# Performance work log

Hardware: AMD Instinct MI355X
Metric: run time of the kernel (lower is better)

## Reference

```python
import jax, jax.numpy as jnp
import numpy as np

B, N, E, F, H, L = 64, 1024, 32768, 128, 32, 2
K = N // 2          # topk ratio 0.5 (fixed in source forward)
NB = 5              # num_neighbors: point cloud points per node
CF, P = 5, 50       # PI channels (filtration methods), PI_dim
OUT = 2

def gcn_conv(x, src, dst, emask, W, b, n):
    # PyG GCNConv: project first, symmetric norm with self-loops; emask zeroes filtered edges
    h = x @ W
    deg = jax.ops.segment_sum(emask, dst, num_segments=n) + 1.0
    dinv = jax.lax.rsqrt(deg)
    coef = (dinv[src] * dinv[dst] * emask)[:, None]
    agg = jax.ops.segment_sum(h[src] * coef, dst, num_segments=n)
    return agg + h * (dinv * dinv)[:, None] + b

def tcl(t, A, Bf, C):
    # Tensor Contraction Layer: mode-1/2/3 factor contraction
    return jnp.einsum('bijk,pi,qj,rk->bpqr', t, A, Bf, C)

def mlp2(h, Wa, ba, Wb, bb):
    return jax.nn.relu(h @ Wa + ba) @ Wb + bb

def setup_inputs():
    key = jax.random.key(0)
    ks = jax.random.split(key, 32)
    s = 0.05
    return {
        'x1': jax.random.normal(ks[0], (B, N, F), jnp.float32),
        'edge_index1': jax.random.randint(ks[1], (B, 2, E), 0, N),
        'PI1': jax.random.uniform(ks[2], (B, CF, P, P), dtype=jnp.float32),
        'x2': jax.random.normal(ks[3], (B, N, F), jnp.float32),
        'edge_index2': jax.random.randint(ks[4], (B, 2, E), 0, N),
        'PI2': jax.random.uniform(ks[5], (B, CF, P, P), dtype=jnp.float32),
        'W_score': jax.random.normal(ks[6], (F, NB * 2)) * s,
        'b_score': jnp.zeros((NB * 2,)),
        'W_gcn0': jax.random.normal(ks[7], (F, H)) * s,
        'b_gcn0': jnp.zeros((H,)),
        'Wm0a': jax.random.normal(ks[8], (H, H)) * s,
        'bm0a': jnp.zeros((H,)),
        'Wm0b': jax.random.normal(ks[9], (H, H * H)) * s,
        'bm0b': jnp.zeros((H * H,)),
        'W_gcn1': jax.random.normal(ks[10], (H * H, H)) * s,
        'b_gcn1': jnp.zeros((H,)),
        'Wm1a': jax.random.normal(ks[11], (H, H)) * s,
        'bm1a': jnp.zeros((H,)),
        'Wm1b': jax.random.normal(ks[12], (H, H * H)) * s,
        'bm1b': jnp.zeros((H * H,)),
        'F0': jax.random.normal(ks[13], (H, L)) * s,
        'F1': jax.random.normal(ks[14], (H, H)) * s,
        'F2': jax.random.normal(ks[15], (H, H)) * s,
        'K_conv': jax.random.normal(ks[16], (H, CF, 2, 2)) * s,
        'b_conv': jnp.zeros((H,)),
        'G0': jax.random.normal(ks[17], (H, H)) * s,
        'G1': jax.random.normal(ks[18], (H, P // 2)) * s,
        'G2': jax.random.normal(ks[19], (H, P // 2)) * s,
        'H0': jax.random.normal(ks[20], (2 * H, 2 * H)) * s,
        'H1': jax.random.normal(ks[21], (H, H)) * s,
        'H2': jax.random.normal(ks[22], (H, H)) * s,
        'Wo1': jax.random.normal(ks[23], (H, H)) * s,
        'bo1': jnp.zeros((H,)),
        'Wo2': jax.random.normal(ks[24], (H, OUT)) * s,
        'bo2': jnp.zeros((OUT,)),
    }

def reference(x1, edge_index1, PI1, x2, edge_index2, PI2, W_score, b_score,
              W_gcn0, b_gcn0, Wm0a, bm0a, Wm0b, bm0b,
              W_gcn1, b_gcn1, Wm1a, bm1a, Wm1b, bm1b,
              F0, F1, F2, K_conv, b_conv, G0, G1, G2,
              H0, H1, H2, Wo1, bo1, Wo2, bo2):
    ones = jnp.ones((E,), jnp.float32)

    def pool_one(xg, s_, d_):
        # score_node_layer -> point cloud -> lifespan score -> topk(0.5) -> filter_adj
        emb = gcn_conv(xg, s_, d_, ones, W_score, b_score, N)
        pc = emb.reshape(N, NB, 2)
        score = jnp.abs(pc[..., 1] - pc[..., 0]).sum(-1)
        _, perm = jax.lax.top_k(score, K)
        newidx = jnp.full((N,), -1).at[perm].set(jnp.arange(K))
        r, c = newidx[s_], newidx[d_]
        valid = (r >= 0) & (c >= 0)
        return xg[perm], jnp.where(valid, r, 0), jnp.where(valid, c, 0), valid.astype(jnp.float32)

    def branch(x, ei, PI):
        src, dst = ei[:, 0, :], ei[:, 1, :]
        xp, psrc, pdst, em = jax.vmap(pool_one)(x, src, dst)
        conv0 = jax.vmap(lambda h, s_, d_, m: gcn_conv(h, s_, d_, m, W_gcn0, b_gcn0, K))
        conv1 = jax.vmap(lambda h, s_, d_, m: gcn_conv(h, s_, d_, m, W_gcn1, b_gcn1, K))
        h1 = mlp2(conv0(xp, psrc, pdst, em), Wm0a, bm0a, Wm0b, bm0b)   # [B,K,H*H]
        h2 = mlp2(conv1(h1, psrc, pdst, em), Wm1a, bm1a, Wm1b, bm1b)   # [B,K,H*H]
        g = jnp.stack([h1.mean(1), h2.mean(1)], axis=1).reshape(B, L, H, H)
        gcn_t = tcl(g, F0, F1, F2)                                      # [B,H,H,H]
        pe = jax.lax.conv_general_dilated(PI, K_conv, (2, 2), 'VALID',
                                          dimension_numbers=('NCHW', 'OIHW', 'NCHW'))
        pe = jax.nn.relu(pe + b_conv[None, :, None, None])              # [B,H,25,25]
        pi_t = tcl(pe, G0, G1, G2)                                      # [B,H,H,H]
        fused = tcl(jnp.concatenate([gcn_t, pi_t], axis=1), H0, H1, H2) # [B,2H,H,H]
        pooled = fused.mean(axis=(1, 3))                                # [B,H]
        return jax.nn.relu(pooled @ Wo1 + bo1) @ Wo2 + bo2              # [B,OUT]

    return jnp.stack([branch(x1, edge_index1, PI1), branch(x2, edge_index2, PI2)])
```

## Files before the change

kernel.cpp:

```cpp
#include <hip/hip_runtime.h>
#include <cstdint>


constexpr int B_ = 64, N_ = 1024, E_ = 32768, F_ = 128, H_ = 32;
constexpr int CF_ = 5, P_ = 50, K_ = 512, G_ = 128, PO = 25;

constexpr size_t WS_SRCS  = 0;
constexpr size_t WS_ONODE = WS_SRCS + (size_t)G_*(E_/2);
constexpr size_t WS_VDEG  = WS_ONODE + (size_t)G_*K_;
constexpr size_t WS_EOFF  = WS_VDEG + (size_t)G_*(K_/2);
constexpr size_t WS_DINV  = WS_EOFF + (size_t)G_*K_;
constexpr size_t WS_GA    = WS_DINV + (size_t)G_*K_;
constexpr size_t WS_GC    = WS_GA + (size_t)G_*K_*H_;
constexpr size_t WS_PM0   = WS_GC + (size_t)G_*K_*H_;
constexpr size_t WS_PM1   = WS_PM0 + (size_t)G_*64;
constexpr size_t WS_PPI   = WS_PM1 + (size_t)G_*64;
constexpr size_t WS_F0V   = WS_PPI + (size_t)G_*32;
constexpr size_t WS_B01   = WS_F0V + 32;
constexpr size_t WS_C0B   = WS_B01 + 32;
constexpr size_t WS_C1B   = WS_C0B + 32;
constexpr size_t WS_W01   = WS_C1B + 32;
constexpr size_t WS_P0B   = WS_W01 + 1024;
constexpr size_t WS_P1B   = WS_P0B + 1024;

constexpr size_t WS_DSC   = WS_GC;

static __device__ __forceinline__ int swzf4(int row, int c4) {
  return row*32 + (((c4) ^ ((row >> 2) & 7)) << 2);
}

__global__ __launch_bounds__(512, 4) void kA_pre(
    const float* __restrict__ x1, const float* __restrict__ x2,
    const float* __restrict__ Wsc,
    const float* __restrict__ F0w, const float* __restrict__ F2w,
    const float* __restrict__ H0w, const float* __restrict__ H2w,
    const float* __restrict__ Wm0b, const float* __restrict__ bm0b,
    const float* __restrict__ Wm1b, const float* __restrict__ bm1b,
    const float* __restrict__ Wg1, float* __restrict__ ws)
{
  __shared__ float SM[640];
  int blk = blockIdx.x, t = threadIdx.x;

  if (blk < 8*G_) {
    int g = blk >> 3, sub = blk & 7, br = g >> 6, b = g & 63;
    const float* xg = (br ? x2 : x1) + (size_t)b*N_*F_;
    float* WdL = SM;
    if (t < F_) {
      #pragma unroll
      for (int j = 0; j < 5; ++j) WdL[t*5+j] = Wsc[t*10+2*j+1] - Wsc[t*10+2*j];
    }
    __syncthreads();
    int row = sub*128 + (t >> 2), q = t & 3;
    const float4* xr = (const float4*)(xg + (size_t)row*F_);
    float acc[5] = {};
    #pragma unroll
    for (int i = 0; i < 8; ++i) {
      int k4 = q + 4*i;
      float4 v = xr[k4];
      const float* w = &WdL[k4*20];
      #pragma unroll
      for (int j = 0; j < 5; ++j)
        acc[j] += v.x*w[j] + v.y*w[5+j] + v.z*w[10+j] + v.w*w[15+j];
    }
    #pragma unroll
    for (int j = 0; j < 5; ++j) {
      acc[j] += __shfl_xor(acc[j], 1, 4);
      acc[j] += __shfl_xor(acc[j], 2, 4);
    }
    if (q == 0) {
      float* o = ws + WS_DSC + ((size_t)g*N_ + row)*5;
      #pragma unroll
      for (int j = 0; j < 5; ++j) o[j] = acc[j];
    }
    return;
  }

  int blk2 = blk - 8*G_;
  if (blk2 == 0) {
    float* h0mS = SM;
    if (t < 32) { float s = 0.f; for (int qq = 0; qq < 64; ++qq) s += H0w[qq*64+t]; h0mS[t] = s*(1.f/64.f); }
    __syncthreads();
    if (t < 2) { float s = 0.f; for (int p = 0; p < 32; ++p) s += F0w[p*2+t]*h0mS[p]; ws[WS_F0V+t] = s; }
  } else if (blk2 <= 32) {
    int kk = blk2 - 1;
    int ol = t >> 4, seg = t & 15;
    const float4* ar = (const float4*)(Wm0b + (size_t)kk*1024 + seg*64);
    float s = 0.f;
    #pragma unroll
    for (int i = 0; i < 16; ++i) {
      float4 a = ar[i];
      int tt = seg*64 + i*4;
      s += a.x*Wg1[(tt+0)*32 + ol] + a.y*Wg1[(tt+1)*32 + ol]
         + a.z*Wg1[(tt+2)*32 + ol] + a.w*Wg1[(tt+3)*32 + ol];
    }
    s += __shfl_xor(s, 1, 16);
    s += __shfl_xor(s, 2, 16);
    s += __shfl_xor(s, 4, 16);
    s += __shfl_xor(s, 8, 16);
    if (seg == 0) ws[WS_W01 + kk*32 + ol] = s;
  } else if (blk2 == 33) {
    float* red = SM;
    int j = t & 31, seg = t >> 5;
    float s = 0.f;
    #pragma unroll
    for (int i = 0; i < 64; ++i) {
      int k = seg*64 + i;
      s += bm0b[k]*Wg1[k*32 + j];
    }
    red[seg*32 + j] = s;
    __syncthreads();
    if (t < 32) {
      float a = 0.f;
      #pragma unroll
      for (int q = 0; q < 16; ++q) a += red[q*32 + t];
      ws[WS_B01 + t] = a;
    }
  } else {
    const float* Wb = (blk2 == 34) ? Wm0b : Wm1b;
    const float* bb = (blk2 == 34) ? bm0b : bm1b;
    size_t dstP = (blk2 == 34) ? WS_P0B : WS_P1B;
    size_t dstC = (blk2 == 34) ? WS_C0B : WS_C1B;
    float* h2mL = SM;
    float* f2vL = SM + 32;
    if (t < 32) { float s = 0.f; for (int r = 0; r < 32; ++r) s += H2w[r*32+t]; h2mL[t] = s*(1.f/32.f); }
    __syncthreads();
    if (t < 32) { float s = 0.f; for (int r = 0; r < 32; ++r) s += F2w[r*32+t]*h2mL[r]; f2vL[t] = s; }
    __syncthreads();
    if (t < 256) {
      #pragma unroll
      for (int q = 0; q < 4; ++q) {
        int e = t*4 + q;
        int k = e >> 5, c = e & 31;
        float s = 0.f;
        #pragma unroll
        for (int kp = 0; kp < 32; ++kp) s += Wb[k*1024 + c*32 + kp]*f2vL[kp];
        ws[dstP + e] = s;
      }
    }
    if (t < 32) {
      float s = 0.f;
      #pragma unroll
      for (int kp = 0; kp < 32; ++kp) s += bb[t*32+kp]*f2vL[kp];
      ws[dstC+t] = s;
    }
  }
}

__global__ __launch_bounds__(256, 4) void kPI(
    const float* __restrict__ PI1, const float* __restrict__ PI2,
    const float* __restrict__ Kc, const float* __restrict__ bc,
    const float* __restrict__ G0w, const float* __restrict__ G2w,
    const float* __restrict__ H0w, const float* __restrict__ H2w,
    float* __restrict__ ws)
{
  int g = blockIdx.x, br = g >> 6, b = g & 63;
  const float* pig = (br ? PI2 : PI1) + (size_t)b*CF_*P_*P_;
  __shared__ float PIt[CF_*P_*P_];
  __shared__ float KcL[H_*CF_*4];
  __shared__ float bcL[H_], g0L[H_], g2L[PO], h2L[H_], hhL[H_];
  int t = threadIdx.x;
  for (int i = t; i < CF_*P_*P_; i += 256) PIt[i] = pig[i];
  for (int i = t; i < H_*CF_*4; i += 256) KcL[i] = Kc[i];
  if (t < 32) {
    bcL[t] = bc[t];
    float s = 0.f;
    for (int qq = 0; qq < 64; ++qq) s += H0w[qq*64 + 32 + t];
    hhL[t] = s * (1.f/64.f);
  }
  if (t >= 64 && t < 96) {
    int r = t - 64;
    float s = 0.f;
    for (int rr = 0; rr < 32; ++rr) s += H2w[rr*32 + r];
    h2L[r] = s * (1.f/32.f);
  }
  __syncthreads();
  if (t < 32) { float s = 0.f; for (int p = 0; p < 32; ++p) s += G0w[p*32+t]*hhL[p]; g0L[t] = s; }
  if (t >= 64 && t < 64+PO) {
    int kp = t - 64;
    float s = 0.f;
    for (int r = 0; r < 32; ++r) s += G2w[r*25+kp]*h2L[r];
    g2L[kp] = s;
  }
  __syncthreads();
  int jp = t >> 3, sub = t & 7;
  float acc = 0.f;
  if (jp < PO) {
    for (int i = sub; i < H_; i += 8) {
      const float* kcp = &KcL[i*20];
      float bi = bcL[i], gi = g0L[i];
      for (int kp = 0; kp < PO; ++kp) {
        float v = bi;
        #pragma unroll
        for (int c = 0; c < CF_; ++c) {
          const float* pp = &PIt[c*2500 + (2*jp)*50 + 2*kp];
          v += pp[0]*kcp[c*4+0] + pp[1]*kcp[c*4+1] + pp[50]*kcp[c*4+2] + pp[51]*kcp[c*4+3];
        }
        acc += fmaxf(v, 0.f) * gi * g2L[kp];
      }
    }
  }
  #pragma unroll
  for (int d = 4; d > 0; d >>= 1) acc += __shfl_down(acc, d, 8);
  if (sub == 0 && jp < PO) ws[WS_PPI + (size_t)g*32 + jp] = acc;
}

__global__ __launch_bounds__(1024, 4) void kBS(
    const int* __restrict__ ei1, const int* __restrict__ ei2,
    const float* __restrict__ bsc, float* __restrict__ ws)
{
  int g = blockIdx.x, br = g >> 6, b = g & 63;
  const int* ei  = (br ? ei2 : ei1) + (size_t)b*2*E_;
  const int* src = ei;
  const int* dst = ei + E_;
  int* onodeg = (int*)ws + WS_ONODE + (size_t)g*K_;
  uint16_t* vdegg = (uint16_t*)(ws + WS_VDEG) + (size_t)g*K_;
  int* ceoffg = (int*)ws + WS_EOFF + (size_t)g*K_;
  float* dinvg = ws + WS_DINV + (size_t)g*K_;
  uint16_t* csrc = (uint16_t*)(ws + WS_SRCS) + (size_t)g*E_;

  __shared__ uint16_t srcL[E_];
  __shared__ float DscL[N_*5];
  __shared__ float dinvF[N_];
  __shared__ int fbL[N_];
  __shared__ int fillL[N_];
  __shared__ int nidxL[N_];
  __shared__ int seoffL[K_];
  __shared__ int vdegL[K_];
  __shared__ int ceoffL[K_];
  __shared__ int hist[256], hsum[256];
  __shared__ int wtot[16], wbase[16], wsum[16];
  __shared__ int remL, dstarL;

  int t = threadIdx.x;
  { const float* Dg = ws + WS_DSC + (size_t)g*N_*5;
    for (int i = t; i < N_*5; i += 1024) DscL[i] = Dg[i]; }
  fillL[t] = 0;
  if (t == 0) remL = K_;
  __syncthreads();

  for (int i = 0; i < E_/1024; ++i) {
    int d = dst[t + i*1024];
    atomicAdd(&fillL[d], 1);
  }
  __syncthreads();

  int c = fillL[t];
  int lane = t & 63, w = t >> 6;
  int x = c;
  #pragma unroll
  for (int s = 1; s < 64; s <<= 1) {
    int v = __shfl_up(x, s);
    if (lane >= s) x += v;
  }
  if (lane == 63) wsum[w] = x;
  __syncthreads();
  if (w == 0 && lane < 16) {
    int y = wsum[lane];
    #pragma unroll
    for (int s = 1; s < 16; s <<= 1) {
      int v = __shfl_up(y, s, 16);
      if (lane >= s) y += v;
    }
    wsum[lane] = y;
  }
  __syncthreads();
  int off0 = ((w == 0) ? 0 : wsum[w-1]) + x - c;
  int off1 = off0 + c;
  fbL[t] = off0;
  dinvF[t] = rsqrtf((float)c + 1.0f);
  fillL[t] = 0;
  __syncthreads();

  for (int i = 0; i < E_/1024; ++i) {
    int e = t + i*1024;
    int d = dst[e], s = src[e];
    int pos = fbL[d] + atomicAdd(&fillL[d], 1);
    srcL[pos] = (uint16_t)s;
  }
  __syncthreads();

  uint32_t key;
  {
    float agg[5] = {};
    for (int e = off0; e < off1; ++e) {
      int s = srcL[e];
      float dvs = dinvF[s];
      const float* hr = &DscL[s*5];
      #pragma unroll
      for (int j = 0; j < 5; ++j) agg[j] += hr[j]*dvs;
    }
    float dv = dinvF[t];
    const float* hn = &DscL[t*5];
    float sc = 0.f;
    #pragma unroll
    for (int j = 0; j < 5; ++j)
      sc += fabsf(dv*(agg[j] + dv*hn[j]) + (bsc[2*j+1] - bsc[2*j]));
    key = __float_as_uint(sc);
  }
  __syncthreads();

  uint32_t pref = 0, prefMask = 0;
  #pragma unroll
  for (int pass = 0; pass < 4; ++pass) {
    int shift = 24 - 8*pass;
    if (t < 256) hist[t] = 0;
    __syncthreads();
    bool cand = (key & prefMask) == pref;
    if (cand) atomicAdd(&hist[(key >> shift) & 255], 1);
    __syncthreads();
    if (t < 256) hsum[t] = hist[t];
    __syncthreads();
    for (int s = 1; s < 256; s <<= 1) {
      int v = 0;
      if (t < 256) v = hsum[t] + ((t + s < 256) ? hsum[t + s] : 0);
      __syncthreads();
      if (t < 256) hsum[t] = v;
      __syncthreads();
    }
    int rem = remL;
    if (t < 256) {
      int above = (t == 255) ? 0 : hsum[t+1];
      if (hsum[t] >= rem && above < rem) dstarL = t;
    }
    __syncthreads();
    int ds = dstarL;
    if (t == 0) remL = rem - ((ds == 255) ? 0 : hsum[ds+1]);
    pref |= (uint32_t)ds << shift;
    prefMask |= 0xFFu << shift;
    __syncthreads();
  }
  uint32_t T = pref;
  int r = remL;

  bool eq = (key == T);
  uint64_t mEq = __ballot(eq);
  int lpEq = (int)__popcll(mEq & ((1ull << lane) - 1));
  if (lane == 0) wtot[w] = (int)__popcll(mEq);
  __syncthreads();
  if (t == 0) { int a = 0; for (int q = 0; q < 16; ++q) { wbase[q] = a; a += wtot[q]; } }
  __syncthreads();
  bool sel = (key > T) || (eq && (wbase[w] + lpEq) < r);
  __syncthreads();
  uint64_t mS = __ballot(sel);
  int lpS = (int)__popcll(mS & ((1ull << lane) - 1));
  if (lane == 0) wtot[w] = (int)__popcll(mS);
  __syncthreads();
  if (t == 0) { int a = 0; for (int q = 0; q < 16; ++q) { wbase[q] = a; a += wtot[q]; } }
  __syncthreads();
  int rank = wbase[w] + lpS;
  nidxL[t] = sel ? rank : -1;
  if (sel) onodeg[rank] = t;
  __syncthreads();

  if (sel) {
    int c2 = 0;
    for (int e = off0; e < off1; ++e) {
      int m = nidxL[srcL[e]];
      if (m >= 0) srcL[off0 + (c2++)] = (uint16_t)m;
    }
    vdegL[rank] = c2;
    seoffL[rank] = off0;
  }
  __syncthreads();

  int vv = 0, xx = 0, w2 = t >> 6;
  if (t < K_) {
    vv = vdegL[t]; xx = vv;
    int l2 = t & 63;
    #pragma unroll
    for (int s = 1; s < 64; s <<= 1) {
      int v = __shfl_up(xx, s);
      if (l2 >= s) xx += v;
    }
    if (l2 == 63) wsum[w2] = xx;
  }
  __syncthreads();
  if (t == 0) { int run = 0; for (int q = 0; q < 8; ++q) { int tm = wsum[q]; wsum[q] = run; run += tm; } }
  __syncthreads();
  if (t < K_) {
    int ce = wsum[w2] + xx - vv;
    ceoffL[t] = ce;
    ceoffg[t] = ce;
    vdegg[t] = (uint16_t)vv;
    dinvg[t] = rsqrtf((float)vv + 1.0f);
  }
  __syncthreads();

  if (t < K_) {
    int s0 = seoffL[t], n = vdegL[t], d0 = ceoffL[t];
    for (int i = 0; i < n; ++i) csrc[d0 + i] = srcL[s0 + i];
  }
}

static __device__ __forceinline__ void mmA(
    const float* __restrict__ S, const float* __restrict__ Wp,
    float (&acc)[4][4], int it, int jt)
{
  const int i0 = it*4, swa = it & 7;
  #pragma unroll
  for (int kv = 0; kv < 8; ++kv) {
    float4 w0 = *(const float4*)&Wp[(kv*4+0)*36 + jt*4];
    float4 w1 = *(const float4*)&Wp[(kv*4+1)*36 + jt*4];
    float4 w2 = *(const float4*)&Wp[(kv*4+2)*36 + jt*4];
    float4 w3 = *(const float4*)&Wp[(kv*4+3)*36 + jt*4];
    #pragma unroll
    for (int d = 0; d < 4; ++d) {
      float4 a = *(const float4*)&S[(i0+d)*32 + ((kv ^ swa) << 2)];
      acc[d][0] += a.x*w0.x + a.y*w1.x + a.z*w2.x + a.w*w3.x;
      acc[d][1] += a.x*w0.y + a.y*w1.y + a.z*w2.y + a.w*w3.y;
      acc[d][2] += a.x*w0.z + a.y*w1.z + a.z*w2.z + a.w*w3.z;
      acc[d][3] += a.x*w0.w + a.y*w1.w + a.z*w2.w + a.w*w3.w;
    }
  }
}

__global__ __launch_bounds__(512, 4) void kG1(
    const float* __restrict__ x1, const float* __restrict__ x2,
    const float* __restrict__ Wg0, float* __restrict__ ws)
{
  int g = blockIdx.x, half = blockIdx.y, br = g >> 6, b = g & 63;
  const float* xg = (br ? x2 : x1) + (size_t)b*N_*F_;
  const int* onodeg = (const int*)ws + WS_ONODE + (size_t)g*K_ + half*256;
  const float* dinvg = ws + WS_DINV + (size_t)g*K_ + half*256;
  float* gAg = ws + WS_GA + (size_t)g*K_*H_ + (size_t)half*256*H_;

  __shared__ float wbuf[F_*36];
  __shared__ int   onodeL[256];
  __shared__ float dinvL[256];

  int t = threadIdx.x;
  for (int i = t; i < F_*H_; i += 512) wbuf[(i >> 5)*36 + (i & 31)] = Wg0[i];
  if (t < 256) { onodeL[t] = onodeg[t]; dinvL[t] = dinvg[t]; }
  __syncthreads();

  const int it = t >> 3, jt = t & 7;
  const int i0 = it*4;
  const float* xr0 = xg + (size_t)onodeL[i0+0]*F_;
  const float* xr1 = xg + (size_t)onodeL[i0+1]*F_;
  const float* xr2 = xg + (size_t)onodeL[i0+2]*F_;
  const float* xr3 = xg + (size_t)onodeL[i0+3]*F_;
  float acc[4][4] = {};
  for (int k4 = 0; k4 < 32; ++k4) {
    float4 w0 = *(const float4*)&wbuf[(k4*4+0)*36 + jt*4];
    float4 w1 = *(const float4*)&wbuf[(k4*4+1)*36 + jt*4];
    float4 w2 = *(const float4*)&wbuf[(k4*4+2)*36 + jt*4];
    float4 w3 = *(const float4*)&wbuf[(k4*4+3)*36 + jt*4];
    float4 a;
    a = *(const float4*)(xr0 + k4*4);
    acc[0][0]+=a.x*w0.x+a.y*w1.x+a.z*w2.x+a.w*w3.x; acc[0][1]+=a.x*w0.y+a.y*w1.y+a.z*w2.y+a.w*w3.y;
    acc[0][2]+=a.x*w0.z+a.y*w1.z+a.z*w2.z+a.w*w3.z; acc[0][3]+=a.x*w0.w+a.y*w1.w+a.z*w2.w+a.w*w3.w;
    a = *(const float4*)(xr1 + k4*4);
    acc[1][0]+=a.x*w0.x+a.y*w1.x+a.z*w2.x+a.w*w3.x; acc[1][1]+=a.x*w0.y+a.y*w1.y+a.z*w2.y+a.w*w3.y;
    acc[1][2]+=a.x*w0.z+a.y*w1.z+a.z*w2.z+a.w*w3.z; acc[1][3]+=a.x*w0.w+a.y*w1.w+a.z*w2.w+a.w*w3.w;
    a = *(const float4*)(xr2 + k4*4);
    acc[2][0]+=a.x*w0.x+a.y*w1.x+a.z*w2.x+a.w*w3.x; acc[2][1]+=a.x*w0.y+a.y*w1.y+a.z*w2.y+a.w*w3.y;
    acc[2][2]+=a.x*w0.z+a.y*w1.z+a.z*w2.z+a.w*w3.z; acc[2][3]+=a.x*w0.w+a.y*w1.w+a.z*w2.w+a.w*w3.w;
    a = *(const float4*)(xr3 + k4*4);
    acc[3][0]+=a.x*w0.x+a.y*w1.x+a.z*w2.x+a.w*w3.x; acc[3][1]+=a.x*w0.y+a.y*w1.y+a.z*w2.y+a.w*w3.y;
    acc[3][2]+=a.x*w0.z+a.y*w1.z+a.z*w2.z+a.w*w3.z; acc[3][3]+=a.x*w0.w+a.y*w1.w+a.z*w2.w+a.w*w3.w;
  }
  #pragma unroll
  for (int d = 0; d < 4; ++d) {
    int row = i0 + d;
    float rs = dinvL[row];
    float4 o; o.x=acc[d][0]*rs; o.y=acc[d][1]*rs; o.z=acc[d][2]*rs; o.w=acc[d][3]*rs;
    *(float4*)&gAg[row*32 + jt*4] = o;
  }
}

static __device__ __forceinline__ void convG(
    const float* __restrict__ gS, float* __restrict__ cbuf,
    const float* __restrict__ bias, const float* __restrict__ dinvL,
    const int* __restrict__ eoffL, const int* __restrict__ vcntL,
    const uint16_t* __restrict__ srcS, int half, int t)
{
  int ddl = t & 255, hc = t >> 8;
  int dd = half*256 + ddl;
  int lo = eoffL[ddl], n = vcntL[ddl];
  int c0 = hc*16;
  float4 a0 = {0,0,0,0}, a1 = a0, a2 = a0, a3 = a0;
  for (int i = 0; i < n; ++i) {
    int ss = srcS[lo + i];
    const float* r = gS + ss*32 + c0;
    float4 v;
    v = *(const float4*)(r+0);  a0.x+=v.x; a0.y+=v.y; a0.z+=v.z; a0.w+=v.w;
    v = *(const float4*)(r+4);  a1.x+=v.x; a1.y+=v.y; a1.z+=v.z; a1.w+=v.w;
    v = *(const float4*)(r+8);  a2.x+=v.x; a2.y+=v.y; a2.z+=v.z; a2.w+=v.w;
    v = *(const float4*)(r+12); a3.x+=v.x; a3.y+=v.y; a3.z+=v.z; a3.w+=v.w;
  }
  { const float* r = gS + dd*32 + c0;
    float4 v;
    v = *(const float4*)(r+0);  a0.x+=v.x; a0.y+=v.y; a0.z+=v.z; a0.w+=v.w;
    v = *(const float4*)(r+4);  a1.x+=v.x; a1.y+=v.y; a1.z+=v.z; a1.w+=v.w;
    v = *(const float4*)(r+8);  a2.x+=v.x; a2.y+=v.y; a2.z+=v.z; a2.w+=v.w;
    v = *(const float4*)(r+12); a3.x+=v.x; a3.y+=v.y; a3.z+=v.z; a3.w+=v.w; }
  float dvd = dinvL[ddl];
  float4 r0, r1, r2, r3;
  r0.x = dvd*a0.x + bias[c0+0];  r0.y = dvd*a0.y + bias[c0+1];
  r0.z = dvd*a0.z + bias[c0+2];  r0.w = dvd*a0.w + bias[c0+3];
  r1.x = dvd*a1.x + bias[c0+4];  r1.y = dvd*a1.y + bias[c0+5];
  r1.z = dvd*a1.z + bias[c0+6];  r1.w = dvd*a1.w + bias[c0+7];
  r2.x = dvd*a2.x + bias[c0+8];  r2.y = dvd*a2.y + bias[c0+9];
  r2.z = dvd*a2.z + bias[c0+10]; r2.w = dvd*a2.w + bias[c0+11];
  r3.x = dvd*a3.x + bias[c0+12]; r3.y = dvd*a3.y + bias[c0+13];
  r3.z = dvd*a3.z + bias[c0+14]; r3.w = dvd*a3.w + bias[c0+15];
  int g4 = hc*4;
  *(float4*)&cbuf[swzf4(ddl, g4+0)] = r0;
  *(float4*)&cbuf[swzf4(ddl, g4+1)] = r1;
  *(float4*)&cbuf[swzf4(ddl, g4+2)] = r2;
  *(float4*)&cbuf[swzf4(ddl, g4+3)] = r3;
}

__global__ __launch_bounds__(512, 4) void kG2(
    const float* __restrict__ bg0,
    const float* __restrict__ Wm0a, const float* __restrict__ bm0a,
    float* __restrict__ ws)
{
  int g = blockIdx.x, half = blockIdx.y;
  const float* gAg = ws + WS_GA + (size_t)g*K_*H_;
  float* gCg = ws + WS_GC + (size_t)g*K_*H_;
  const uint16_t* srcS = (const uint16_t*)(ws + WS_SRCS) + (size_t)g*E_;
  const int* eoffg = (const int*)ws + WS_EOFF + (size_t)g*K_ + half*256;
  const uint16_t* vdegg = (const uint16_t*)(ws + WS_VDEG) + (size_t)g*K_ + half*256;
  const float* dinvg = ws + WS_DINV + (size_t)g*K_ + half*256;

  __shared__ float cbufA[256*32];
  __shared__ float cbufB[256*32];
  __shared__ float wA[32*36];
  __shared__ float wB[32*36];
  __shared__ float scrP[64*33];
  __shared__ int   eoffL[256];
  __shared__ int   vcntL[256];
  __shared__ float dinvL[256];

  int t = threadIdx.x;
  for (int i = t; i < 1024; i += 512) {
    int k = i >> 5, j = i & 31;
    wA[k*36+j] = Wm0a[i];
    wB[k*36+j] = ws[WS_W01 + i];
  }
  if (t < 256) { eoffL[t] = eoffg[t]; vcntL[t] = vdegg[t]; dinvL[t] = dinvg[t]; }
  __syncthreads();

  convG(gAg, cbufA, bg0, dinvL, eoffL, vcntL, srcS, half, t);
  __syncthreads();

  const int it = t >> 3, jt = t & 7;
  float acc[4][4] = {};
  mmA(cbufA, wA, acc, it, jt);
  {
    float b0 = bm0a[jt*4+0], b1 = bm0a[jt*4+1], b2 = bm0a[jt*4+2], b3 = bm0a[jt*4+3];
    float cp0=0.f, cp1=0.f, cp2=0.f, cp3=0.f;
    #pragma unroll
    for (int d = 0; d < 4; ++d) {
      float v0=fmaxf(acc[d][0]+b0,0.f), v1=fmaxf(acc[d][1]+b1,0.f);
      float v2=fmaxf(acc[d][2]+b2,0.f), v3=fmaxf(acc[d][3]+b3,0.f);
      cp0+=v0; cp1+=v1; cp2+=v2; cp3+=v3;
      float4 o; o.x=v0; o.y=v1; o.z=v2; o.w=v3;
      *(float4*)&cbufB[swzf4(it*4+d, jt)] = o;
    }
    scrP[it*33 + jt*4+0] = cp0; scrP[it*33 + jt*4+1] = cp1;
    scrP[it*33 + jt*4+2] = cp2; scrP[it*33 + jt*4+3] = cp3;
  }
  __syncthreads();

  if (t < 32) {
    float s = 0.f;
    #pragma unroll
    for (int q = 0; q < 64; ++q) s += scrP[q*33 + t];
    ws[WS_PM0 + (size_t)g*64 + half*32 + t] = s;
  }

  float acc2[4][4] = {};
  mmA(cbufB, wB, acc2, it, jt);
  {
    float b0 = ws[WS_B01+jt*4+0], b1 = ws[WS_B01+jt*4+1];
    float b2 = ws[WS_B01+jt*4+2], b3 = ws[WS_B01+jt*4+3];
    #pragma unroll
    for (int d = 0; d < 4; ++d) {
      int row = it*4 + d;
      float rs = dinvL[row];
      float4 o;
      o.x=(acc2[d][0]+b0)*rs; o.y=(acc2[d][1]+b1)*rs;
      o.z=(acc2[d][2]+b2)*rs; o.w=(acc2[d][3]+b3)*rs;
      *(float4*)&gCg[(half*256+row)*32 + jt*4] = o;
    }
  }
}

__global__ __launch_bounds__(512, 4) void kG4(
    const float* __restrict__ bg1,
    const float* __restrict__ Wm1a, const float* __restrict__ bm1a,
    float* __restrict__ ws)
{
  int g = blockIdx.x, half = blockIdx.y;
  const float* gCg = ws + WS_GC + (size_t)g*K_*H_;
  const uint16_t* srcS = (const uint16_t*)(ws + WS_SRCS) + (size_t)g*E_;
  const int* eoffg = (const int*)ws + WS_EOFF + (size_t)g*K_ + half*256;
  const uint16_t* vdegg = (const uint16_t*)(ws + WS_VDEG) + (size_t)g*K_ + half*256;
  const float* dinvg = ws + WS_DINV + (size_t)g*K_ + half*256;

  __shared__ float cbufA[256*32];
  __shared__ float wA[32*36];
  __shared__ float scrP[64*33];
  __shared__ int   eoffL[256];
  __shared__ int   vcntL[256];
  __shared__ float dinvL[256];

  int t = threadIdx.x;
  for (int i = t; i < 1024; i += 512) wA[(i>>5)*36 + (i&31)] = Wm1a[i];
  if (t < 256) { eoffL[t] = eoffg[t]; vcntL[t] = vdegg[t]; dinvL[t] = dinvg[t]; }
  __syncthreads();

  convG(gCg, cbufA, bg1, dinvL, eoffL, vcntL, srcS, half, t);
  __syncthreads();

  const int it = t >> 3, jt = t & 7;
  float acc[4][4] = {};
  mmA(cbufA, wA, acc, it, jt);
  {
    float b0 = bm1a[jt*4+0], b1 = bm1a[jt*4+1], b2 = bm1a[jt*4+2], b3 = bm1a[jt*4+3];
    float cp0=0.f, cp1=0.f, cp2=0.f, cp3=0.f;
    #pragma unroll
    for (int d = 0; d < 4; ++d) {
      cp0 += fmaxf(acc[d][0]+b0,0.f); cp1 += fmaxf(acc[d][1]+b1,0.f);
      cp2 += fmaxf(acc[d][2]+b2,0.f); cp3 += fmaxf(acc[d][3]+b3,0.f);
    }
    scrP[it*33 + jt*4+0] = cp0; scrP[it*33 + jt*4+1] = cp1;
    scrP[it*33 + jt*4+2] = cp2; scrP[it*33 + jt*4+3] = cp3;
  }
  __syncthreads();

  if (t < 32) {
    float s = 0.f;
    #pragma unroll
    for (int q = 0; q < 64; ++q) s += scrP[q*33 + t];
    ws[WS_PM1 + (size_t)g*64 + half*32 + t] = s;
  }
}

__global__ __launch_bounds__(64) void k5_final(
    const float* __restrict__ F1w, const float* __restrict__ G1w,
    const float* __restrict__ H1w, const float* __restrict__ Wo1,
    const float* __restrict__ bo1, const float* __restrict__ Wo2,
    const float* __restrict__ bo2, const float* __restrict__ ws,
    float* __restrict__ out)
{
  int g = blockIdx.x, t = threadIdx.x;
  __shared__ float mr0[32], mr1[32], AL[32], TL[32], pl[32], zl[32], ppiL[PO];
  if (t < 32) {
    mr0[t] = (ws[WS_PM0 + (size_t)g*64 + t] + ws[WS_PM0 + (size_t)g*64 + 32 + t]) * (1.f/512.f);
    mr1[t] = (ws[WS_PM1 + (size_t)g*64 + t] + ws[WS_PM1 + (size_t)g*64 + 32 + t]) * (1.f/512.f);
  }
  if (t >= 32 && t < 32+PO) ppiL[t-32] = ws[WS_PPI + (size_t)g*32 + (t-32)];
  __syncthreads();
  float f00 = ws[WS_F0V], f01 = ws[WS_F0V+1];
  if (t < 32) {
    float s0 = ws[WS_C0B + t], s1 = ws[WS_C1B + t];
    for (int k = 0; k < 32; ++k) {
      s0 += mr0[k]*ws[WS_P0B + k*32 + t];
      s1 += mr1[k]*ws[WS_P1B + k*32 + t];
    }
    AL[t] = f00*s0 + f01*s1;
  }
  __syncthreads();
  if (t < 32) {
    float s = 0.f;
    for (int jp = 0; jp < 32; ++jp) s += F1w[t*32+jp]*AL[jp];
    for (int jp = 0; jp < PO; ++jp) s += G1w[t*25+jp]*ppiL[jp];
    TL[t] = s;
  }
  __syncthreads();
  if (t < 32) {
    float s = 0.f;
    for (int j = 0; j < 32; ++j) s += H1w[t*32+j]*TL[j];
    pl[t] = s;
  }
  __syncthreads();
  if (t < 32) {
    float s = bo1[t];
    for (int j = 0; j < 32; ++j) s += pl[j]*Wo1[j*32+t];
    zl[t] = fmaxf(s, 0.f);
  }
  __syncthreads();
  if (t < 2) {
    float s = bo2[t];
    for (int q = 0; q < 32; ++q) s += zl[q]*Wo2[q*2+t];
    int br = g >> 6, b = g & 63;
    out[br*(B_*2) + b*2 + t] = s;
  }
}

extern "C" void kernel_launch(void* const* d_in, const int* in_sizes, int n_in,
                              void* d_out, int out_size, void* d_ws, size_t ws_size,
                              hipStream_t stream) {
  (void)in_sizes; (void)n_in; (void)out_size; (void)ws_size;
  const float* x1      = (const float*)d_in[0];
  const int*   ei1     = (const int*)  d_in[1];
  const float* PI1     = (const float*)d_in[2];
  const float* x2      = (const float*)d_in[3];
  const int*   ei2     = (const int*)  d_in[4];
  const float* PI2     = (const float*)d_in[5];
  const float* W_score = (const float*)d_in[6];
  const float* b_score = (const float*)d_in[7];
  const float* W_gcn0  = (const float*)d_in[8];
  const float* b_gcn0  = (const float*)d_in[9];
  const float* Wm0a    = (const float*)d_in[10];
  const float* bm0a    = (const float*)d_in[11];
  const float* Wm0b    = (const float*)d_in[12];
  const float* bm0b    = (const float*)d_in[13];
  const float* W_gcn1  = (const float*)d_in[14];
  const float* b_gcn1  = (const float*)d_in[15];
  const float* Wm1a    = (const float*)d_in[16];
  const float* bm1a    = (const float*)d_in[17];
  const float* Wm1b    = (const float*)d_in[18];
  const float* bm1b    = (const float*)d_in[19];
  const float* F0w     = (const float*)d_in[20];
  const float* F1w     = (const float*)d_in[21];
  const float* F2w     = (const float*)d_in[22];
  const float* Kc      = (const float*)d_in[23];
  const float* bc      = (const float*)d_in[24];
  const float* G0w     = (const float*)d_in[25];
  const float* G1w     = (const float*)d_in[26];
  const float* G2w     = (const float*)d_in[27];
  const float* H0w     = (const float*)d_in[28];
  const float* H1w     = (const float*)d_in[29];
  const float* H2w     = (const float*)d_in[30];
  const float* Wo1     = (const float*)d_in[31];
  const float* bo1     = (const float*)d_in[32];
  const float* Wo2     = (const float*)d_in[33];
  const float* bo2     = (const float*)d_in[34];
  float* ws  = (float*)d_ws;
  float* out = (float*)d_out;

  kA_pre<<<8*G_ + 36, 512, 0, stream>>>(x1, x2, W_score,
                                        F0w, F2w, H0w, H2w,
                                        Wm0b, bm0b, Wm1b, bm1b, W_gcn1, ws);
  kPI<<<G_, 256, 0, stream>>>(PI1, PI2, Kc, bc, G0w, G2w, H0w, H2w, ws);
  kBS<<<G_, 1024, 0, stream>>>(ei1, ei2, b_score, ws);
  kG1<<<dim3(G_, 2), 512, 0, stream>>>(x1, x2, W_gcn0, ws);
  kG2<<<dim3(G_, 2), 512, 0, stream>>>(b_gcn0, Wm0a, bm0a, ws);
  kG4<<<dim3(G_, 2), 512, 0, stream>>>(b_gcn1, Wm1a, bm1a, ws);
  k5_final<<<G_, 64, 0, stream>>>(F1w, G1w, H1w, Wo1, bo1, Wo2, bo2, ws, out);
}
```

Measured before the change: 188.9 us.

## Reparallelize PI conv over output positions and use wave-level suffix scan in top-k

The PI kernel now assigns each thread a conv output position, caches its 2x2x5 input patch in registers, loops over all 32 channels, and reduces rows through shared scratch. Before, 8 threads per row each walked 25 columns and 4 channels, and only 200 of 256 threads did work. The H0/H2 column means are now computed cooperatively by all threads with shuffles instead of 32 serial threads each. In kBS, the 8-step block-wide Hillis-Steele suffix scan with barriers is replaced by a single-wavefront shuffle scan, and the histogram reset is folded into the selection step to remove barriers per radix pass.

```diff
diff --git a/kernel.cpp b/kernel.cpp
--- a/kernel.cpp
+++ b/kernel.cpp
@@ -158,21 +158,29 @@
   __shared__ float PIt[CF_*P_*P_];
   __shared__ float KcL[H_*CF_*4];
   __shared__ float bcL[H_], g0L[H_], g2L[PO], h2L[H_], hhL[H_];
+  __shared__ float scr[640];
   int t = threadIdx.x;
   for (int i = t; i < CF_*P_*P_; i += 256) PIt[i] = pig[i];
   for (int i = t; i < H_*CF_*4; i += 256) KcL[i] = Kc[i];
-  if (t < 32) {
-    bcL[t] = bc[t];
-    float s = 0.f;
-    for (int qq = 0; qq < 64; ++qq) s += H0w[qq*64 + 32 + t];
-    hhL[t] = s * (1.f/64.f);
-  }
-  if (t >= 64 && t < 96) {
-    int r = t - 64;
-    float s = 0.f;
-    for (int rr = 0; rr < 32; ++rr) s += H2w[rr*32 + r];
-    h2L[r] = s * (1.f/32.f);
-  }
+  {
+    int p = t >> 3, s = t & 7;
+    float v = 0.f;
+    #pragma unroll
+    for (int q = 0; q < 8; ++q) v += H0w[(s + q*8)*64 + 32 + p];
+    #pragma unroll
+    for (int d = 4; d > 0; d >>= 1) v += __shfl_down(v, d, 8);
+    if (s == 0) hhL[p] = v * (1.f/64.f);
+  }
+  {
+    int r = t >> 3, s = t & 7;
+    float v = 0.f;
+    #pragma unroll
+    for (int q = 0; q < 4; ++q) v += H2w[(s + q*8)*32 + r];
+    #pragma unroll
+    for (int d = 4; d > 0; d >>= 1) v += __shfl_down(v, d, 8);
+    if (s == 0) h2L[r] = v * (1.f/32.f);
+  }
+  if (t < 32) bcL[t] = bc[t];
   __syncthreads();
   if (t < 32) { float s = 0.f; for (int p = 0; p < 32; ++p) s += G0w[p*32+t]*hhL[p]; g0L[t] = s; }
   if (t >= 64 && t < 64+PO) {
@@ -182,26 +190,32 @@
     g2L[kp] = s;
   }
   __syncthreads();
-  int jp = t >> 3, sub = t & 7;
-  float acc = 0.f;
-  if (jp < PO) {
-    for (int i = sub; i < H_; i += 8) {
+  for (int pos = t; pos < PO*PO; pos += 256) {
+    int jp = pos / PO, kp = pos - jp*PO;
+    float p00[CF_], p01[CF_], p10[CF_], p11[CF_];
+    #pragma unroll
+    for (int c = 0; c < CF_; ++c) {
+      const float* q = &PIt[c*2500 + (2*jp)*50 + 2*kp];
+      p00[c] = q[0]; p01[c] = q[1]; p10[c] = q[50]; p11[c] = q[51];
+    }
+    float acc = 0.f;
+    for (int i = 0; i < H_; ++i) {
+      float v = bcL[i];
       const float* kcp = &KcL[i*20];
-      float bi = bcL[i], gi = g0L[i];
-      for (int kp = 0; kp < PO; ++kp) {
-        float v = bi;
-        #pragma unroll
-        for (int c = 0; c < CF_; ++c) {
-          const float* pp = &PIt[c*2500 + (2*jp)*50 + 2*kp];
-          v += pp[0]*kcp[c*4+0] + pp[1]*kcp[c*4+1] + pp[50]*kcp[c*4+2] + pp[51]*kcp[c*4+3];
-        }
-        acc += fmaxf(v, 0.f) * gi * g2L[kp];
-      }
-    }
-  }
-  #pragma unroll
-  for (int d = 4; d > 0; d >>= 1) acc += __shfl_down(acc, d, 8);
-  if (sub == 0 && jp < PO) ws[WS_PPI + (size_t)g*32 + jp] = acc;
+      #pragma unroll
+      for (int c = 0; c < CF_; ++c)
+        v += p00[c]*kcp[c*4+0] + p01[c]*kcp[c*4+1] + p10[c]*kcp[c*4+2] + p11[c]*kcp[c*4+3];
+      acc += fmaxf(v, 0.f) * g0L[i];
+    }
+    scr[pos] = acc * g2L[kp];
+  }
+  __syncthreads();
+  if (t < PO) {
+    float s = 0.f;
+    #pragma unroll
+    for (int k = 0; k < PO; ++k) s += scr[t*PO + k];
+    ws[WS_PPI + (size_t)g*32 + t] = s;
+  }
 }
 
 __global__ __launch_bounds__(1024, 4) void kBS(
@@ -235,6 +249,7 @@
   { const float* Dg = ws + WS_DSC + (size_t)g*N_*5;
     for (int i = t; i < N_*5; i += 1024) DscL[i] = Dg[i]; }
   fillL[t] = 0;
+  if (t < 256) hist[t] = 0;
   if (t == 0) remL = K_;
   __syncthreads();
 
@@ -303,32 +318,37 @@
   #pragma unroll
   for (int pass = 0; pass < 4; ++pass) {
     int shift = 24 - 8*pass;
-    if (t < 256) hist[t] = 0;
-    __syncthreads();
     bool cand = (key & prefMask) == pref;
     if (cand) atomicAdd(&hist[(key >> shift) & 255], 1);
     __syncthreads();
-    if (t < 256) hsum[t] = hist[t];
+    if (w == 0) {
+      int base = lane*4;
+      int h0 = hist[base+0], h1 = hist[base+1], h2 = hist[base+2], h3 = hist[base+3];
+      int suf = h0 + h1 + h2 + h3;
+      #pragma unroll
+      for (int sh = 1; sh < 64; sh <<= 1) {
+        int v = __shfl_down(suf, sh);
+        if (lane + sh < 64) suf += v;
+      }
+      hsum[base+0] = suf;
+      hsum[base+1] = suf - h0;
+      hsum[base+2] = suf - h0 - h1;
+      hsum[base+3] = suf - h0 - h1 - h2;
+    }
     __syncthreads();
-    for (int s = 1; s < 256; s <<= 1) {
-      int v = 0;
-      if (t < 256) v = hsum[t] + ((t + s < 256) ? hsum[t + s] : 0);
-      __syncthreads();
-      if (t < 256) hsum[t] = v;
-      __syncthreads();
-    }
     int rem = remL;
     if (t < 256) {
       int above = (t == 255) ? 0 : hsum[t+1];
       if (hsum[t] >= rem && above < rem) dstarL = t;
+      hist[t] = 0;
     }
     __syncthreads();
     int ds = dstarL;
     if (t == 0) remL = rem - ((ds == 255) ? 0 : hsum[ds+1]);
     pref |= (uint32_t)ds << shift;
     prefMask |= 0xFFu << shift;
-    __syncthreads();
-  }
+  }
+  __syncthreads();
   uint32_t T = pref;
   int r = remL;
 
```

Result: faster. 174.1 us (-7.8%).
